# Performance work log

Measured on AMD Instinct MI355X. Metric: run time of the kernel, lower is better.

The kernel has to match this reference:

```python
import jax, jax.numpy as jnp
import numpy as np

N = 20000      # nodes
E = 320000     # edges (avg degree 16)
C = 64         # channels per degree
H = 8          # attention heads
DIM1 = 3       # degree-1 representation dim (2*1+1)
NUM_FEATURES = C * 1 + C * 3  # key_fiber.num_features = 256


def setup_inputs() -> dict:
    key = jax.random.key(0)
    ks = jax.random.split(key, 7)
    return {
        "value_0": jax.random.normal(ks[0], (E, C, 1), dtype=jnp.float32),
        "value_1": jax.random.normal(ks[1], (E, C, DIM1), dtype=jnp.float32),
        "key_0": jax.random.normal(ks[2], (E, C, 1), dtype=jnp.float32),
        "key_1": jax.random.normal(ks[3], (E, C, DIM1), dtype=jnp.float32),
        "query_0": jax.random.normal(ks[4], (N, C, 1), dtype=jnp.float32),
        "query_1": jax.random.normal(ks[5], (N, C, DIM1), dtype=jnp.float32),
        "dst": jax.random.randint(ks[6], (E,), 0, N),
    }


def _to_heads(f0, f1):
    # Fiber.to_attention_heads: per degree [n, C, dim] -> [n, H, (C//H)*dim], concat on last dim
    n = f0.shape[0]
    return jnp.concatenate([f0.reshape(n, H, -1), f1.reshape(n, H, -1)], axis=-1)


def reference(value_0, value_1, key_0, key_1, query_0, query_1, dst):
    k = _to_heads(key_0, key_1)        # [E, H, Dk]
    q = _to_heads(query_0, query_1)    # [N, H, Dk]
    # dgl.ops.e_dot_v: dot edge key with destination-node query, then scale
    logits = jnp.einsum('ehd,ehd->eh', k, q[dst]) / np.float32(np.sqrt(NUM_FEATURES))
    edge_prelogits = logits            # returned pre-softmax (scaled) as in original
    # edge_softmax over incoming edges of each destination node, per head
    m = jax.ops.segment_max(logits, dst, num_segments=N)           # [N, H]
    w = jnp.exp(logits - m[dst])                                   # [E, H]
    denom = jax.ops.segment_sum(w, dst, num_segments=N)            # [N, H]
    alpha = w / denom[dst]                                         # [E, H]

    def agg(v, dim):
        # value view: [E, H, C//H, dim]; weighted copy_e_sum -> [N, C, dim]
        vh = v.reshape(E, H, C // H, dim)
        out = jax.ops.segment_sum(alpha[:, :, None, None] * vh, dst, num_segments=N)
        return out.reshape(N, C, dim)

    out_0 = agg(value_0, 1)
    out_1 = agg(value_1, DIM1)
    return out_0, out_1, edge_prelogits
```

## Files before the change

### kernel.cpp

```cpp
#include <hip/hip_runtime.h>

#define N_NODES 20000
#define N_EDGES 320000
#define NEGF   -1e30f


__global__ __launch_bounds__(256) void k_zero(int* __restrict__ counts)
{
    int n = blockIdx.x * 256 + threadIdx.x;
    if (n < N_NODES) counts[n] = 0;
}

__global__ __launch_bounds__(256) void k_count(
    const int* __restrict__ dst, int* __restrict__ counts)
{
    int e = blockIdx.x * 256 + threadIdx.x;
    if (e < N_EDGES) atomicAdd(&counts[dst[e]], 1);
}

__global__ __launch_bounds__(1024) void k_scan(
    const int* __restrict__ counts, int* __restrict__ offsets,
    int* __restrict__ cursor)
{
    __shared__ int sm[1024];
    int t = threadIdx.x;
    int base = t * 20;
    int local[20];
    int s = 0;
    if (base < N_NODES) {
#pragma unroll
        for (int i = 0; i < 20; ++i) { local[i] = counts[base + i]; s += local[i]; }
    }
    sm[t] = s; __syncthreads();
    for (int off = 1; off < 1024; off <<= 1) {
        int x = (t >= off) ? sm[t - off] : 0;
        __syncthreads();
        sm[t] += x;
        __syncthreads();
    }
    int run = sm[t] - s;
    if (base < N_NODES) {
#pragma unroll
        for (int i = 0; i < 20; ++i) {
            offsets[base + i] = run; cursor[base + i] = run; run += local[i];
        }
    }
    if (t == 0) offsets[N_NODES] = N_EDGES;
}

__global__ __launch_bounds__(256) void k_logits(
    const float* __restrict__ k0, const float* __restrict__ k1,
    const float* __restrict__ q0, const float* __restrict__ q1,
    const int* __restrict__ dst, float* __restrict__ logits,
    int* __restrict__ cursor, int* __restrict__ bucket)
{
    int t = blockIdx.x * 256 + threadIdx.x;
    if (t >= N_EDGES * 8) return;
    int e = t >> 3, h = t & 7;
    int d = dst[e];

    const float4* k0v = (const float4*)(k0 + (size_t)e * 64  + h * 8);
    const float4* q0v = (const float4*)(q0 + (size_t)d * 64  + h * 8);
    const float4* k1v = (const float4*)(k1 + (size_t)e * 192 + h * 24);
    const float4* q1v = (const float4*)(q1 + (size_t)d * 192 + h * 24);

    float s = 0.f;
#pragma unroll
    for (int i = 0; i < 2; ++i) {
        float4 a = k0v[i], b = q0v[i];
        s += a.x * b.x + a.y * b.y + a.z * b.z + a.w * b.w;
    }
#pragma unroll
    for (int i = 0; i < 6; ++i) {
        float4 a = k1v[i], b = q1v[i];
        s += a.x * b.x + a.y * b.y + a.z * b.z + a.w * b.w;
    }
    logits[t] = s * 0.0625f;
    if (h == 0) {
        int pos = atomicAdd(&cursor[d], 1);
        bucket[pos] = e;
    }
}

__global__ __launch_bounds__(256) void k_agg(
    const float* __restrict__ v0, const float* __restrict__ v1,
    const float* __restrict__ logits, const int* __restrict__ offsets,
    const int* __restrict__ bucket,
    float* __restrict__ out0, float* __restrict__ out1)
{
    __shared__ float xb[4][512];
    int w = threadIdx.x >> 6;
    int l = threadIdx.x & 63;
    int node = blockIdx.x * 4 + w;
    if (node >= N_NODES) return;
    float* X = xb[w];

    int rs = offsets[node], re = offsets[node + 1];
    int deg = re - rs;
    int h = l & 7, slot8 = l >> 3;

    float M = NEGF, S = 0.f;
    for (int base = 0; base < deg; base += 8) {
        int s = base + slot8;
        float x = NEGF;
        if (s < deg) {
            int e = bucket[rs + s];
            x = logits[(size_t)e * 8 + h];
            if (s < 64) X[s * 8 + h] = x;
        }
        float Mn = fmaxf(M, x);
        S = S * __expf(M - Mn) + ((s < deg) ? __expf(x - Mn) : 0.f);
        M = Mn;
    }
    for (int mask = 8; mask < 64; mask <<= 1) {
        float Mo = __shfl_xor(M, mask);
        float So = __shfl_xor(S, mask);
        float Mn = fmaxf(M, Mo);
        S = S * __expf(M - Mn) + So * __expf(Mo - Mn);
        M = Mn;
    }
    float rinv = (S > 0.f) ? 1.f / S : 0.f;

    int degc = deg < 64 ? deg : 64;
    for (int base = 0; base < degc; base += 8) {
        int s = base + slot8;
        if (s < degc) X[s * 8 + h] = __expf(X[s * 8 + h] - M) * rinv;
    }

    int s2 = l >> 4;
    int c  = l & 15;
    int hv0  = c >> 1;
    int hv1a = c / 6;
    int hv1b = (c + 16) / 6;
    int hv1c = (c + 32) / 6;
    float M0 = __shfl(M, hv0),  R0 = __shfl(rinv, hv0);
    float Ma = __shfl(M, hv1a), Ra = __shfl(rinv, hv1a);
    float Mb = __shfl(M, hv1b), Rb = __shfl(rinv, hv1b);
    float Mc = __shfl(M, hv1c), Rc = __shfl(rinv, hv1c);

    float4 a0  = {0,0,0,0}, a1a = {0,0,0,0}, a1b = {0,0,0,0}, a1c = {0,0,0,0};
    for (int base = 0; base < deg; base += 4) {
        int s = base + s2;
        bool ok = s < deg;
        int e = bucket[rs + (ok ? s : deg - 1)];
        float al0, ala, alb, alc;
        if (s < 64) {
            al0 = X[s * 8 + hv0];
            ala = X[s * 8 + hv1a];
            alb = X[s * 8 + hv1b];
            alc = X[s * 8 + hv1c];
        } else {
            const float* lr = logits + (size_t)e * 8;
            al0 = __expf(lr[hv0]  - M0) * R0;
            ala = __expf(lr[hv1a] - Ma) * Ra;
            alb = __expf(lr[hv1b] - Mb) * Rb;
            alc = __expf(lr[hv1c] - Mc) * Rc;
        }
        if (!ok) { al0 = ala = alb = alc = 0.f; }
        const float4* r0 = (const float4*)(v0 + (size_t)e * 64);
        const float4* r1 = (const float4*)(v1 + (size_t)e * 192);
        float4 p0 = r0[c];
        float4 pa = r1[c];
        float4 pb = r1[c + 16];
        float4 pc = r1[c + 32];
        a0.x  += al0 * p0.x; a0.y  += al0 * p0.y; a0.z  += al0 * p0.z; a0.w  += al0 * p0.w;
        a1a.x += ala * pa.x; a1a.y += ala * pa.y; a1a.z += ala * pa.z; a1a.w += ala * pa.w;
        a1b.x += alb * pb.x; a1b.y += alb * pb.y; a1b.z += alb * pb.z; a1b.w += alb * pb.w;
        a1c.x += alc * pc.x; a1c.y += alc * pc.y; a1c.z += alc * pc.z; a1c.w += alc * pc.w;
    }
#pragma unroll
    for (int mask = 16; mask < 64; mask <<= 1) {
        a0.x  += __shfl_xor(a0.x,  mask); a0.y  += __shfl_xor(a0.y,  mask);
        a0.z  += __shfl_xor(a0.z,  mask); a0.w  += __shfl_xor(a0.w,  mask);
        a1a.x += __shfl_xor(a1a.x, mask); a1a.y += __shfl_xor(a1a.y, mask);
        a1a.z += __shfl_xor(a1a.z, mask); a1a.w += __shfl_xor(a1a.w, mask);
        a1b.x += __shfl_xor(a1b.x, mask); a1b.y += __shfl_xor(a1b.y, mask);
        a1b.z += __shfl_xor(a1b.z, mask); a1b.w += __shfl_xor(a1b.w, mask);
        a1c.x += __shfl_xor(a1c.x, mask); a1c.y += __shfl_xor(a1c.y, mask);
        a1c.z += __shfl_xor(a1c.z, mask); a1c.w += __shfl_xor(a1c.w, mask);
    }
    if (l < 16) {
        float4* o0 = (float4*)(out0 + (size_t)node * 64);
        float4* o1 = (float4*)(out1 + (size_t)node * 192);
        o0[c]      = a0;
        o1[c]      = a1a;
        o1[c + 16] = a1b;
        o1[c + 32] = a1c;
    }
}

extern "C" void kernel_launch(void* const* d_in, const int* in_sizes, int n_in,
                              void* d_out, int out_size, void* d_ws, size_t ws_size,
                              hipStream_t stream) {
    const float* v0 = (const float*)d_in[0];
    const float* v1 = (const float*)d_in[1];
    const float* k0 = (const float*)d_in[2];
    const float* k1 = (const float*)d_in[3];
    const float* q0 = (const float*)d_in[4];
    const float* q1 = (const float*)d_in[5];
    const int*  dst = (const int*)d_in[6];

    float* out0   = (float*)d_out;
    float* out1   = out0 + (size_t)N_NODES * 64;
    float* logits = out1 + (size_t)N_NODES * 192;

    int* wsI     = (int*)d_ws;
    int* counts  = wsI;
    int* offsets = wsI + 20000;
    int* cursor  = wsI + 40064;
    int* bucket  = wsI + 60192;

    k_zero   <<<79,    256,  0, stream>>>(counts);
    k_count  <<<1250,  256,  0, stream>>>(dst, counts);
    k_scan   <<<1,     1024, 0, stream>>>(counts, offsets, cursor);
    k_logits <<<10000, 256,  0, stream>>>(k0, k1, q0, q1, dst, logits, cursor, bucket);
    k_agg    <<<5000,  256,  0, stream>>>(v0, v1, logits, offsets, bucket, out0, out1);
}
```

Baseline: 217.1 us.

## Fuse logit computation into per-node aggregation kernel with shared-memory query

Moves the key-query dot products from a separate edge-parallel kernel into the node-parallel aggregation kernel, loading each node's query once into shared memory. The separate logits readback is gone and the bucket fill becomes its own light kernel. It saves the logits round trip and the repeated gathers of the query rows. The trade-off is that edge keys are now gathered per node in a less coalesced, degree-imbalanced loop. The early return was removed to allow __syncthreads; the grid exactly covers 20000 nodes, so this is safe.

```diff
diff --git a/kernel.cpp b/kernel.cpp
--- a/kernel.cpp
+++ b/kernel.cpp
@@ -48,68 +48,70 @@
     if (t == 0) offsets[N_NODES] = N_EDGES;
 }
 
-__global__ __launch_bounds__(256) void k_logits(
+__global__ __launch_bounds__(256) void k_fill(
+    const int* __restrict__ dst, int* __restrict__ cursor, int* __restrict__ bucket)
+{
+    int e = blockIdx.x * 256 + threadIdx.x;
+    if (e >= N_EDGES) return;
+    int d = dst[e];
+    int pos = atomicAdd(&cursor[d], 1);
+    bucket[pos] = e;
+}
+
+__global__ __launch_bounds__(256) void k_fused(
+    const float* __restrict__ v0, const float* __restrict__ v1,
     const float* __restrict__ k0, const float* __restrict__ k1,
     const float* __restrict__ q0, const float* __restrict__ q1,
-    const int* __restrict__ dst, float* __restrict__ logits,
-    int* __restrict__ cursor, int* __restrict__ bucket)
-{
-    int t = blockIdx.x * 256 + threadIdx.x;
-    if (t >= N_EDGES * 8) return;
-    int e = t >> 3, h = t & 7;
-    int d = dst[e];
-
-    const float4* k0v = (const float4*)(k0 + (size_t)e * 64  + h * 8);
-    const float4* q0v = (const float4*)(q0 + (size_t)d * 64  + h * 8);
-    const float4* k1v = (const float4*)(k1 + (size_t)e * 192 + h * 24);
-    const float4* q1v = (const float4*)(q1 + (size_t)d * 192 + h * 24);
-
-    float s = 0.f;
-#pragma unroll
-    for (int i = 0; i < 2; ++i) {
-        float4 a = k0v[i], b = q0v[i];
-        s += a.x * b.x + a.y * b.y + a.z * b.z + a.w * b.w;
-    }
-#pragma unroll
-    for (int i = 0; i < 6; ++i) {
-        float4 a = k1v[i], b = q1v[i];
-        s += a.x * b.x + a.y * b.y + a.z * b.z + a.w * b.w;
-    }
-    logits[t] = s * 0.0625f;
-    if (h == 0) {
-        int pos = atomicAdd(&cursor[d], 1);
-        bucket[pos] = e;
-    }
-}
-
-__global__ __launch_bounds__(256) void k_agg(
-    const float* __restrict__ v0, const float* __restrict__ v1,
-    const float* __restrict__ logits, const int* __restrict__ offsets,
-    const int* __restrict__ bucket,
-    float* __restrict__ out0, float* __restrict__ out1)
+    const int* __restrict__ offsets, const int* __restrict__ bucket,
+    float* __restrict__ logits, float* __restrict__ out0, float* __restrict__ out1)
 {
     __shared__ float xb[4][512];
+    __shared__ float qs[4][256];
     int w = threadIdx.x >> 6;
     int l = threadIdx.x & 63;
     int node = blockIdx.x * 4 + w;
-    if (node >= N_NODES) return;
     float* X = xb[w];
+    float* Q = qs[w];
 
     int rs = offsets[node], re = offsets[node + 1];
     int deg = re - rs;
     int h = l & 7, slot8 = l >> 3;
 
+    {
+        float4* Qv = (float4*)Q;
+        if (l < 16) Qv[l] = ((const float4*)(q0 + (size_t)node * 64))[l];
+        else        Qv[l] = ((const float4*)(q1 + (size_t)node * 192))[l - 16];
+    }
+    __syncthreads();
+
+    const float4* Qh0 = (const float4*)(Q + h * 8);
+    const float4* Qh1 = (const float4*)(Q + 64 + h * 24);
     float M = NEGF, S = 0.f;
     for (int base = 0; base < deg; base += 8) {
         int s = base + slot8;
+        bool ok = s < deg;
         float x = NEGF;
-        if (s < deg) {
+        if (ok) {
             int e = bucket[rs + s];
-            x = logits[(size_t)e * 8 + h];
+            const float4* kk0 = (const float4*)(k0 + (size_t)e * 64  + h * 8);
+            const float4* kk1 = (const float4*)(k1 + (size_t)e * 192 + h * 24);
+            float acc = 0.f;
+#pragma unroll
+            for (int i = 0; i < 2; ++i) {
+                float4 a = kk0[i], b = Qh0[i];
+                acc += a.x * b.x + a.y * b.y + a.z * b.z + a.w * b.w;
+            }
+#pragma unroll
+            for (int i = 0; i < 6; ++i) {
+                float4 a = kk1[i], b = Qh1[i];
+                acc += a.x * b.x + a.y * b.y + a.z * b.z + a.w * b.w;
+            }
+            x = acc * 0.0625f;
+            logits[(size_t)e * 8 + h] = x;
             if (s < 64) X[s * 8 + h] = x;
         }
         float Mn = fmaxf(M, x);
-        S = S * __expf(M - Mn) + ((s < deg) ? __expf(x - Mn) : 0.f);
+        S = S * __expf(M - Mn) + (ok ? __expf(x - Mn) : 0.f);
         M = Mn;
     }
     for (int mask = 8; mask < 64; mask <<= 1) {
@@ -126,6 +128,7 @@
         int s = base + slot8;
         if (s < degc) X[s * 8 + h] = __expf(X[s * 8 + h] - M) * rinv;
     }
+    __syncthreads();
 
     int s2 = l >> 4;
     int c  = l & 15;
@@ -210,9 +213,10 @@
     int* cursor  = wsI + 40064;
     int* bucket  = wsI + 60192;
 
-    k_zero   <<<79,    256,  0, stream>>>(counts);
-    k_count  <<<1250,  256,  0, stream>>>(dst, counts);
-    k_scan   <<<1,     1024, 0, stream>>>(counts, offsets, cursor);
-    k_logits <<<10000, 256,  0, stream>>>(k0, k1, q0, q1, dst, logits, cursor, bucket);
-    k_agg    <<<5000,  256,  0, stream>>>(v0, v1, logits, offsets, bucket, out0, out1);
-}
+    k_zero  <<<79,    256,  0, stream>>>(counts);
+    k_count <<<1250,  256,  0, stream>>>(dst, counts);
+    k_scan  <<<1,     1024, 0, stream>>>(counts, offsets, cursor);
+    k_fill  <<<1250,  256,  0, stream>>>(dst, cursor, bucket);
+    k_fused <<<5000,  256,  0, stream>>>(v0, v1, k0, k1, q0, q1,
+                                         offsets, bucket, logits, out0, out1);
+}
```

Result: faster. 204.2 us (-5.9%).
